# Performance work log

Measured on AMD Instinct MI355X. Metric: run time of the kernel, lower is better.

The kernel has to match this reference:

```python
import jax, jax.numpy as jnp
import numpy as np

B, T, D = 4, 2048, 1024
H, Dh = 16, 64
Q_LAT, KV_LAT, O_LAT = 512, 256, 512
ROPE = 32
FFN_RANK, FFN_INTER = 384, 4096
EPS = 1e-6
THETA = 10000.0


def rms_norm(x, w, eps=EPS):
    xf = x.astype(jnp.float32)
    var = jnp.mean(xf * xf, axis=-1, keepdims=True)
    return (w * (xf * jax.lax.rsqrt(var + eps))).astype(x.dtype)


def rotate_half(x):
    x1, x2 = jnp.split(x, 2, axis=-1)
    return jnp.concatenate([-x2, x1], axis=-1)


def setup_inputs() -> dict:
    key = jax.random.key(0)
    ks = jax.random.split(key, 12)
    s = lambda fan_in: 1.0 / np.sqrt(fan_in)
    inp = {
        "hidden_states": jax.random.normal(ks[0], (B, T, D), jnp.float32),
        "ln1_w": jnp.ones((D,), jnp.float32),
        "a_ln_w": jnp.ones((Q_LAT + KV_LAT,), jnp.float32),
        "qkv_a_w": jax.random.normal(ks[1], (D, Q_LAT + KV_LAT), jnp.float32) * s(D),
        "q_b_w": jax.random.normal(ks[2], (Q_LAT, H * Dh), jnp.float32) * s(Q_LAT),
        "kv_b_w": jax.random.normal(ks[3], (KV_LAT, 2 * H * Dh), jnp.float32) * s(KV_LAT),
        "o_a_w": jax.random.normal(ks[4], (H * Dh, O_LAT), jnp.float32) * s(H * Dh),
        "o_b_w": jax.random.normal(ks[5], (O_LAT, D), jnp.float32) * s(O_LAT),
        "ln2_w": jnp.ones((D,), jnp.float32),
        "ffn_in_a": jax.random.normal(ks[6], (D, FFN_RANK), jnp.float32) * s(D),
        "ffn_in_b": jax.random.normal(ks[7], (FFN_RANK, FFN_INTER), jnp.float32) * s(FFN_RANK),
        "ffn_out_a": jax.random.normal(ks[8], (FFN_INTER, FFN_RANK), jnp.float32) * s(FFN_INTER),
        "ffn_out_b": jax.random.normal(ks[9], (FFN_RANK, D), jnp.float32) * s(FFN_RANK),
    }
    # RoPE tables over first ROPE dims of each head
    inv_freq = 1.0 / (THETA ** (np.arange(0, ROPE, 2, dtype=np.float32) / ROPE))
    t = np.arange(T, dtype=np.float32)
    freqs = np.outer(t, inv_freq)                      # [T, ROPE/2]
    emb = np.concatenate([freqs, freqs], axis=-1)      # [T, ROPE]
    inp["cos"] = jnp.asarray(np.cos(emb), jnp.float32)
    inp["sin"] = jnp.asarray(np.sin(emb), jnp.float32)
    return inp


def reference(hidden_states, cos, sin, ln1_w, a_ln_w, qkv_a_w, q_b_w, kv_b_w,
              o_a_w, o_b_w, ln2_w, ffn_in_a, ffn_in_b, ffn_out_a, ffn_out_b):
    x = hidden_states
    # --- MLA attention (pre-norm) ---
    h = rms_norm(x, ln1_w)
    lat = rms_norm(h @ qkv_a_w, a_ln_w)                # [B,T,Q_LAT+KV_LAT]
    q_lat, kv_lat = jnp.split(lat, [Q_LAT], axis=-1)
    q = (q_lat @ q_b_w).reshape(B, T, H, Dh).transpose(0, 2, 1, 3)   # [B,H,T,Dh]
    kv = (kv_lat @ kv_b_w).reshape(B, T, H, 2 * Dh).transpose(0, 2, 1, 3)
    k, v = jnp.split(kv, 2, axis=-1)
    # partial RoPE on first ROPE dims
    c = cos[None, None]; s_ = sin[None, None]          # [1,1,T,ROPE]
    q_r, q_p = q[..., :ROPE], q[..., ROPE:]
    k_r, k_p = k[..., :ROPE], k[..., ROPE:]
    q = jnp.concatenate([q_r * c + rotate_half(q_r) * s_, q_p], axis=-1)
    k = jnp.concatenate([k_r * c + rotate_half(k_r) * s_, k_p], axis=-1)
    scores = jnp.einsum("bhqd,bhkd->bhqk", q, k) * (Dh ** -0.5)
    attn = jax.nn.softmax(scores, axis=-1)
    ctx = jnp.einsum("bhqk,bhkd->bhqd", attn, v)
    ctx = ctx.transpose(0, 2, 1, 3).reshape(B, T, H * Dh)
    attn_out = (ctx @ o_a_w) @ o_b_w                   # output subspace
    x = x + attn_out
    # --- decomposed FFN (pre-norm) ---
    h2 = rms_norm(x, ln2_w)
    ff = jax.nn.gelu((h2 @ ffn_in_a) @ ffn_in_b)
    ff = (ff @ ffn_out_a) @ ffn_out_b
    return x + ff
```

## Files before the change

kernel.cpp:

```cpp
#include <hip/hip_runtime.h>
#include <hip/hip_bf16.h>
#include <stdint.h>

#define NB 4
#define NT 2048
#define ND 1024
#define NH 16
#define NDH 64
#define NQL 512
#define NKVL 256
#define NLAT 768
#define NOLAT 512
#define NFR 384
#define NFI 4096
#define NTOK 8192

typedef unsigned short u16;
typedef __attribute__((ext_vector_type(4))) float f32x4;
typedef __attribute__((ext_vector_type(8))) short s16x8;
typedef __attribute__((ext_vector_type(8))) u16   u16x8;
typedef __attribute__((ext_vector_type(4))) u16   u16x4;

__device__ __forceinline__ float fast_exp2(float x) {
    return __builtin_amdgcn_exp2f(x);
}

__device__ __forceinline__ u16 f2bf(float f) {
    uint32_t u = __float_as_uint(f);
    u = (u + 0x7FFFu + ((u >> 16) & 1u)) >> 16;
    return (u16)u;
}
__device__ __forceinline__ u16 f2bf_fast(float f) {
    return (u16)((__float_as_uint(f) + 0x8000u) >> 16);
}
__device__ __forceinline__ float bf2f(u16 h) {
    return __uint_as_float(((uint32_t)h) << 16);
}

__device__ __forceinline__ void async_cp16(const void* g, void* l) {
    __builtin_amdgcn_global_load_lds(
        (const __attribute__((address_space(1))) void*)g,
        (__attribute__((address_space(3))) void*)l, 16, 0, 0);
}

__device__ __forceinline__ void wait_vm4()   { asm volatile("s_waitcnt vmcnt(4)" ::: "memory"); }
__device__ __forceinline__ void wait_vm0()   { asm volatile("s_waitcnt vmcnt(0)" ::: "memory"); }
__device__ __forceinline__ void wait_lgkm0() { asm volatile("s_waitcnt lgkmcnt(0)" ::: "memory"); }
__device__ __forceinline__ void raw_barrier(){ asm volatile("s_barrier" ::: "memory"); }

struct TDesc { const float* s; u16* d; int K; int N; int tile0; };
struct TPack { TDesc t[9]; };

__global__ __launch_bounds__(256) void k_transpose_all(TPack p)
{
    __shared__ float tile[32][33];
    int bid = blockIdx.x;
    int i = 0;
    #pragma unroll
    for (int j = 1; j < 9; j++) if (bid >= p.t[j].tile0) i = j;
    const float* src = p.t[i].s;
    u16* dst = p.t[i].d;
    int K = p.t[i].K, N = p.t[i].N;
    int local = bid - p.t[i].tile0;
    int nx = N >> 5;
    int n0 = (local % nx) * 32, k0 = (local / nx) * 32;
    int tx = threadIdx.x, ty = threadIdx.y;
    #pragma unroll
    for (int r = 0; r < 32; r += 8)
        tile[ty + r][tx] = src[(size_t)(k0 + ty + r) * N + n0 + tx];
    __syncthreads();
    #pragma unroll
    for (int r = 0; r < 32; r += 8)
        dst[(size_t)(n0 + ty + r) * K + k0 + tx] = f2bf(tile[tx][ty + r]);
}

template<int W>
__global__ __launch_bounds__(256) void k_rmsnorm(
    const float* __restrict__ x, const float* __restrict__ w, u16* __restrict__ out)
{
    constexpr int E = W / 256;
    int row = blockIdx.x, tid = threadIdx.x;
    const float* xr = x + (size_t)row * W;
    float v[E]; float ss = 0.f;
    #pragma unroll
    for (int i = 0; i < E; i++) { v[i] = xr[tid + i * 256]; ss += v[i] * v[i]; }
    #pragma unroll
    for (int m = 1; m < 64; m <<= 1) ss += __shfl_xor(ss, m, 64);
    __shared__ float red[4];
    if ((tid & 63) == 0) red[tid >> 6] = ss;
    __syncthreads();
    ss = red[0] + red[1] + red[2] + red[3];
    float scale = rsqrtf(ss / (float)W + 1e-6f);
    u16* orow = out + (size_t)row * W;
    #pragma unroll
    for (int i = 0; i < E; i++)
        orow[tid + i * 256] = f2bf(w[tid + i * 256] * (v[i] * scale));
}

template<int EPI>
__global__ __launch_bounds__(256) void k_gemm(
    const u16* __restrict__ A, int lda,
    const u16* __restrict__ Bt,
    int M, int N, int K,
    float* __restrict__ outF, u16* __restrict__ outB,
    const float* __restrict__ resid)
{
    __shared__ __align__(16) u16 As[2][4096];
    __shared__ __align__(16) u16 Bs[2][4096];
    int tid = threadIdx.x;
    int w = tid >> 6, lane = tid & 63;
    int m0 = blockIdx.y * 128, n0 = blockIdx.x * 128;
    int wm = w & 1, wn = w >> 1;
    int lr = lane & 15, lq = lane >> 4;

    f32x4 acc[4][4];
    #pragma unroll
    for (int i = 0; i < 4; i++)
        #pragma unroll
        for (int j = 0; j < 4; j++) acc[i][j] = (f32x4)(0.f);

    int ar = tid >> 2;
    int ac = (tid & 3) * 8;
    const u16* Ag = A  + (size_t)(m0 + ar) * lda + ac;
    const u16* Bg = Bt + (size_t)(n0 + ar) * K   + ac;
    int lo = w * 512;

    auto stage = [&](int kt, int s) {
        const u16* a  = Ag + (size_t)kt * 32;
        const u16* bp = Bg + (size_t)kt * 32;
        async_cp16(a,                     &As[s][lo]);
        async_cp16(a + (size_t)64 * lda,  &As[s][lo + 2048]);
        async_cp16(bp,                    &Bs[s][lo]);
        async_cp16(bp + (size_t)64 * K,   &Bs[s][lo + 2048]);
    };

    int nk = K >> 5;
    stage(0, 0);
    stage(1, 1);
    for (int k = 0; k < nk; k++) {
        if (k + 1 < nk) wait_vm4(); else wait_vm0();
        raw_barrier();
        int s = k & 1;
        s16x8 af[4], bfr[4];
        #pragma unroll
        for (int ms = 0; ms < 4; ms++)
            af[ms] = *reinterpret_cast<const s16x8*>(&As[s][(wm * 64 + ms * 16 + lr) * 32 + lq * 8]);
        #pragma unroll
        for (int ns = 0; ns < 4; ns++)
            bfr[ns] = *reinterpret_cast<const s16x8*>(&Bs[s][(wn * 64 + ns * 16 + lr) * 32 + lq * 8]);
        #pragma unroll
        for (int ms = 0; ms < 4; ms++)
            #pragma unroll
            for (int ns = 0; ns < 4; ns++)
                acc[ms][ns] = __builtin_amdgcn_mfma_f32_16x16x32_bf16(af[ms], bfr[ns], acc[ms][ns], 0, 0, 0);
        wait_lgkm0();
        raw_barrier();
        if (k + 2 < nk) stage(k + 2, s);
    }

    #pragma unroll
    for (int ms = 0; ms < 4; ms++) {
        #pragma unroll
        for (int ns = 0; ns < 4; ns++) {
            int col = n0 + wn * 64 + ns * 16 + lr;
            #pragma unroll
            for (int r = 0; r < 4; r++) {
                int row = m0 + wm * 64 + ms * 16 + lq * 4 + r;
                float v = acc[ms][ns][r];
                size_t idx = (size_t)row * N + col;
                if (EPI == 0) {
                    outF[idx] = v;
                } else if (EPI == 1) {
                    outB[idx] = f2bf(v);
                } else if (EPI == 2) {
                    float t = 0.7978845608028654f * (v + 0.044715f * v * v * v);
                    outB[idx] = f2bf(0.5f * v * (1.f + tanhf(t)));
                } else {
                    outF[idx] = v + resid[idx];
                }
            }
        }
    }
}

__global__ __launch_bounds__(256) void k_rope(
    const u16* __restrict__ q, const u16* __restrict__ kv,
    const float* __restrict__ cosb, const float* __restrict__ sinb,
    u16* __restrict__ q_r, u16* __restrict__ k_r)
{
    const float QS = 0.125f * 1.4426950408889634f;
    int idx = blockIdx.x * 256 + threadIdx.x;
    int g = idx & 7;
    int h = (idx >> 3) & 15;
    int t = (idx >> 7) & 2047;
    int b = idx >> 18;
    size_t qsrc = ((size_t)((b * 2048 + t) * 16 + h)) * 64 + g * 8;
    size_t ksrc = ((size_t)((b * 2048 + t) * 16 + h)) * 128 + g * 8;
    u16x8 qa = *(const u16x8*)&q[qsrc];
    u16x8 ka = *(const u16x8*)&kv[ksrc];
    u16x8 qo, ko;
    if (g < 4) {
        int pd = ((g ^ 2) - g) * 8;
        u16x8 qp = *(const u16x8*)&q[qsrc + pd];
        u16x8 kp = *(const u16x8*)&kv[ksrc + pd];
        float sgn = (g < 2) ? -1.f : 1.f;
        const float* cp = &cosb[t * 32 + g * 8];
        const float* sp = &sinb[t * 32 + g * 8];
        #pragma unroll
        for (int j = 0; j < 8; j++) {
            float c = cp[j], s = sp[j];
            qo[j] = f2bf((bf2f(qa[j]) * c + sgn * bf2f(qp[j]) * s) * QS);
            ko[j] = f2bf(bf2f(ka[j]) * c + sgn * bf2f(kp[j]) * s);
        }
    } else {
        #pragma unroll
        for (int j = 0; j < 8; j++) {
            qo[j] = f2bf(bf2f(qa[j]) * QS);
            ko[j] = ka[j];
        }
    }
    size_t dst = ((size_t)(b * 16 + h) * 2048 + t) * 64 + g * 8;
    *(u16x8*)&q_r[dst] = qo;
    *(u16x8*)&k_r[dst] = ko;
}

__global__ __launch_bounds__(256) void k_vtrans(
    const u16* __restrict__ kv, u16* __restrict__ v_t)
{
    __shared__ u16 tile[64][72];
    int bh = blockIdx.y;
    int b = bh >> 4, h = bh & 15;
    int t0 = blockIdx.x * 64;
    int tid = threadIdx.x;
    int r = tid >> 2;
    int c4 = (tid & 3) * 16;
    const u16* src = kv + ((size_t)((b * 2048 + t0 + r) * 16 + h)) * 128 + 64;
    #pragma unroll
    for (int j = 0; j < 16; j += 8)
        *(u16x8*)&tile[r][c4 + j] = *(const u16x8*)&src[c4 + j];
    __syncthreads();
    int dd = tid >> 2;
    u16* dst = v_t + ((size_t)bh * 64 + dd) * 2048 + t0;
    #pragma unroll
    for (int j0 = 0; j0 < 16; j0 += 8) {
        u16x8 vv;
        #pragma unroll
        for (int j = 0; j < 8; j++) vv[j] = tile[c4 + j0 + j][dd];
        *(u16x8*)&dst[c4 + j0] = vv;
    }
}

__global__ __launch_bounds__(256) void k_attn(
    const u16* __restrict__ q_r, const u16* __restrict__ k_r,
    const u16* __restrict__ v_t, u16* __restrict__ ctx)
{
    __shared__ __align__(16) u16 Ks[4096];
    __shared__ __align__(16) u16 Vs[4096];
    __shared__ __align__(16) u16 Ps[4][2048];
    int tid = threadIdx.x, w = tid >> 6, lane = tid & 63;
    int bh = blockIdx.y;
    int b = bh >> 4, h = bh & 15;
    int q0 = blockIdx.x * 128 + w * 32;
    const u16* Qp = q_r + (size_t)bh * 2048 * 64;
    const u16* Kp = k_r + (size_t)bh * 2048 * 64;
    const u16* Vp = v_t + (size_t)bh * 64 * 2048;
    int lr = lane & 15, lq = lane >> 4;
    int rot = (lr * 8) & 63;

    s16x8 qf[2][2];
    #pragma unroll
    for (int qc = 0; qc < 2; qc++)
        #pragma unroll
        for (int kf = 0; kf < 2; kf++)
            qf[qc][kf] = *(const s16x8*)&Qp[(size_t)(q0 + qc * 16 + lr) * 64 + kf * 32 + lq * 8];

    const u16* gstage;
    u16* lstage;
    size_t grow;
    if (w < 2) {
        gstage = Kp + (size_t)(lane >> 2) * 64 + w * 32 + (lane & 3) * 8;
        lstage = Ks + w * 2048;
        grow = 16 * 64;
    } else {
        gstage = Vp + (size_t)(lane >> 2) * 2048 + (w - 2) * 32 + (lane & 3) * 8;
        lstage = Vs + (w - 2) * 2048;
        grow = 16 * 2048;
    }

    float l0 = 0.f, l1 = 0.f;
    f32x4 o[2][4];
    #pragma unroll
    for (int qt = 0; qt < 2; qt++)
        #pragma unroll
        for (int ds = 0; ds < 4; ds++) o[qt][ds] = (f32x4)(0.f);

    u16* Pw = Ps[w];

    for (int kt = 0; kt < 2048; kt += 64) {
        size_t goff = (w < 2) ? (size_t)kt * 64 : (size_t)kt;
        #pragma unroll
        for (int g = 0; g < 4; g++)
            async_cp16(gstage + goff + g * grow, lstage + g * 512);
        __syncthreads();

        f32x4 sc[2][4];
        #pragma unroll
        for (int ns = 0; ns < 4; ns++) {
            s16x8 a0 = *(const s16x8*)&Ks[(ns * 16 + lr) * 32 + lq * 8];
            s16x8 a1 = *(const s16x8*)&Ks[2048 + (ns * 16 + lr) * 32 + lq * 8];
            #pragma unroll
            for (int qc = 0; qc < 2; qc++) {
                f32x4 t = (f32x4)(0.f);
                t = __builtin_amdgcn_mfma_f32_16x16x32_bf16(a0, qf[qc][0], t, 0, 0, 0);
                t = __builtin_amdgcn_mfma_f32_16x16x32_bf16(a1, qf[qc][1], t, 0, 0, 0);
                sc[qc][ns] = t;
            }
        }

        float rs0 = 0.f, rs1 = 0.f;
        #pragma unroll
        for (int ns = 0; ns < 4; ns++) {
            u16x4 pk0, pk1;
            #pragma unroll
            for (int r = 0; r < 4; r++) {
                float p0 = fast_exp2(sc[0][ns][r]);
                float p1 = fast_exp2(sc[1][ns][r]);
                rs0 += p0; rs1 += p1;
                pk0[r] = f2bf_fast(p0);
                pk1[r] = f2bf_fast(p1);
            }
            int c0 = (ns * 16 + lq * 4 + rot) & 63;
            *(u16x4*)&Pw[lr * 64 + c0] = pk0;
            *(u16x4*)&Pw[(16 + lr) * 64 + c0] = pk1;
        }
        rs0 += __shfl_xor(rs0, 16, 64);
        rs0 += __shfl_xor(rs0, 32, 64);
        rs1 += __shfl_xor(rs1, 16, 64);
        rs1 += __shfl_xor(rs1, 32, 64);
        l0 += rs0;
        l1 += rs1;

        #pragma unroll
        for (int kf = 0; kf < 2; kf++) {
            int cr = (kf * 32 + lq * 8 + rot) & 63;
            s16x8 pf0 = *(const s16x8*)&Pw[lr * 64 + cr];
            s16x8 pf1 = *(const s16x8*)&Pw[(16 + lr) * 64 + cr];
            #pragma unroll
            for (int ds = 0; ds < 4; ds++) {
                s16x8 vf = *(const s16x8*)&Vs[kf * 2048 + (ds * 16 + lr) * 32 + lq * 8];
                o[0][ds] = __builtin_amdgcn_mfma_f32_16x16x32_bf16(pf0, vf, o[0][ds], 0, 0, 0);
                o[1][ds] = __builtin_amdgcn_mfma_f32_16x16x32_bf16(pf1, vf, o[1][ds], 0, 0, 0);
            }
        }
        __syncthreads();
    }

    #pragma unroll
    for (int qt = 0; qt < 2; qt++) {
        float lv = qt ? l1 : l0;
        float li[4];
        #pragma unroll
        for (int r = 0; r < 4; r++) li[r] = 1.f / __shfl(lv, lq * 4 + r, 64);
        #pragma unroll
        for (int ds = 0; ds < 4; ds++)
            #pragma unroll
            for (int r = 0; r < 4; r++) {
                int tq = q0 + qt * 16 + lq * 4 + r;
                float v = o[qt][ds][r] * li[r];
                ctx[((size_t)(b * 2048) + tq) * 1024 + h * 64 + ds * 16 + lr] = f2bf(v);
            }
    }
}

extern "C" void kernel_launch(void* const* d_in, const int* in_sizes, int n_in,
                              void* d_out, int out_size, void* d_ws, size_t ws_size,
                              hipStream_t stream) {
    (void)in_sizes; (void)n_in; (void)out_size; (void)ws_size;
    const float* x     = (const float*)d_in[0];
    const float* ln1   = (const float*)d_in[1];
    const float* alnw  = (const float*)d_in[2];
    const float* qkv_a = (const float*)d_in[3];
    const float* q_b   = (const float*)d_in[4];
    const float* kv_b  = (const float*)d_in[5];
    const float* o_a   = (const float*)d_in[6];
    const float* o_b   = (const float*)d_in[7];
    const float* ln2   = (const float*)d_in[8];
    const float* in_a  = (const float*)d_in[9];
    const float* in_b  = (const float*)d_in[10];
    const float* out_a = (const float*)d_in[11];
    const float* out_b = (const float*)d_in[12];
    const float* cosb  = (const float*)d_in[13];
    const float* sinb  = (const float*)d_in[14];
    float* out = (float*)d_out;
    char* ws = (char*)d_ws;

    u16* wqkv = (u16*)(ws);
    u16* wq   = wqkv + 786432;
    u16* wkv  = wq   + 524288;
    u16* woa  = wkv  + 524288;
    u16* wob  = woa  + 524288;
    u16* wia  = wob  + 524288;
    u16* wib  = wia  + 393216;
    u16* woa2 = wib  + 1572864;
    u16* wob2 = woa2 + 1572864;

    float* x2 = (float*)(ws + 13631488);
    char* P = ws + 47185920;
    u16*  hbuf    = (u16*)(P + 0);
    float* lat_raw = (float*)(P + 16777216);
    u16*  lat     = (u16*)(P + 41943040);
    u16*  qbuf    = (u16*)(P + 54525952);
    u16*  kvbuf   = (u16*)(P + 71303168);
    u16*  q_r     = (u16*)(P + 0);
    u16*  k_r     = (u16*)(P + 16777216);
    u16*  v_t     = (u16*)(P + 33554432);
    u16*  ctx     = (u16*)(P + 54525952);
    u16*  t_oa    = (u16*)(P + 71303168);
    u16*  h2      = (u16*)(P + 79691776);
    u16*  t1      = (u16*)(P + 96468992);
    u16*  t2      = (u16*)(P + 0);
    u16*  t3      = (u16*)(P + 67108864);

    TPack tp;
    tp.t[0] = { qkv_a, wqkv, 1024, 768,  0 };
    tp.t[1] = { q_b,   wq,   512,  1024, 768 };
    tp.t[2] = { kv_b,  wkv,  256,  2048, 1280 };
    tp.t[3] = { o_a,   woa,  1024, 512,  1792 };
    tp.t[4] = { o_b,   wob,  512,  1024, 2304 };
    tp.t[5] = { in_a,  wia,  1024, 384,  2816 };
    tp.t[6] = { in_b,  wib,  384,  4096, 3200 };
    tp.t[7] = { out_a, woa2, 4096, 384,  4736 };
    tp.t[8] = { out_b, wob2, 384,  1024, 6272 };
    k_transpose_all<<<6656, dim3(32, 8), 0, stream>>>(tp);

    k_rmsnorm<1024><<<NTOK, 256, 0, stream>>>(x, ln1, hbuf);
    k_gemm<0><<<dim3(6, 64),  256, 0, stream>>>(hbuf, 1024, wqkv, NTOK, 768, 1024, lat_raw, nullptr, nullptr);
    k_rmsnorm<768><<<NTOK, 256, 0, stream>>>(lat_raw, alnw, lat);
    k_gemm<1><<<dim3(8, 64),  256, 0, stream>>>(lat,       768, wq,  NTOK, 1024, 512, nullptr, qbuf,  nullptr);
    k_gemm<1><<<dim3(16, 64), 256, 0, stream>>>(lat + 512, 768, wkv, NTOK, 2048, 256, nullptr, kvbuf, nullptr);
    k_rope<<<4096, 256, 0, stream>>>(qbuf, kvbuf, cosb, sinb, q_r, k_r);
    k_vtrans<<<dim3(32, 64), 256, 0, stream>>>(kvbuf, v_t);
    k_attn<<<dim3(16, 64), 256, 0, stream>>>(q_r, k_r, v_t, ctx);
    k_gemm<1><<<dim3(4, 64),  256, 0, stream>>>(ctx,  1024, woa,  NTOK, 512, 1024, nullptr, t_oa, nullptr);
    k_gemm<3><<<dim3(8, 64),  256, 0, stream>>>(t_oa, 512,  wob,  NTOK, 1024, 512, x2, nullptr, x);
    k_rmsnorm<1024><<<NTOK, 256, 0, stream>>>(x2, ln2, h2);
    k_gemm<1><<<dim3(3, 64),  256, 0, stream>>>(h2, 1024, wia,  NTOK, 384, 1024, nullptr, t1, nullptr);
    k_gemm<2><<<dim3(32, 64), 256, 0, stream>>>(t1, 384,  wib,  NTOK, 4096, 384, nullptr, t2, nullptr);
    k_gemm<1><<<dim3(3, 64),  256, 0, stream>>>(t2, 4096, woa2, NTOK, 384, 4096, nullptr, t3, nullptr);
    k_gemm<3><<<dim3(8, 64),  256, 0, stream>>>(t3, 384,  wob2, NTOK, 1024, 384, out, nullptr, x2);
}
```

Baseline: 562.6 us.

## Fold attention output projections, split-K GEMMs, chunk FFN, double-buffer attention KV

Precomputes the product of o_a and o_b once so the attention output becomes a single 1024x1024 GEMM instead of two chained GEMMs. Adds split-K via blockIdx.z with atomic float accumulation for the narrow-N GEMMs (qkv_a, ffn_in_a, ffn_out_a), using a memset plus conversion kernels. Splits the FFN intermediate into two 2048-wide chunks so the GELU output fits in a smaller, more cache-friendly buffer. Double-buffers the K/V tiles in the attention kernel with async loads. Atomics make the results nondeterministic and change rounding, the folded weight is rounded to bf16 once more, and extra kernels and a memset are added.

```diff
diff --git a/kernel.cpp b/kernel.cpp
--- a/kernel.cpp
+++ b/kernel.cpp
@@ -2,17 +2,6 @@
 #include <hip/hip_bf16.h>
 #include <stdint.h>
 
-#define NB 4
-#define NT 2048
-#define ND 1024
-#define NH 16
-#define NDH 64
-#define NQL 512
-#define NKVL 256
-#define NLAT 768
-#define NOLAT 512
-#define NFR 384
-#define NFI 4096
 #define NTOK 8192
 
 typedef unsigned short u16;
@@ -24,7 +13,6 @@
 __device__ __forceinline__ float fast_exp2(float x) {
     return __builtin_amdgcn_exp2f(x);
 }
-
 __device__ __forceinline__ u16 f2bf(float f) {
     uint32_t u = __float_as_uint(f);
     u = (u + 0x7FFFu + ((u >> 16) & 1u)) >> 16;
@@ -36,20 +24,18 @@
 __device__ __forceinline__ float bf2f(u16 h) {
     return __uint_as_float(((uint32_t)h) << 16);
 }
-
 __device__ __forceinline__ void async_cp16(const void* g, void* l) {
     __builtin_amdgcn_global_load_lds(
         (const __attribute__((address_space(1))) void*)g,
         (__attribute__((address_space(3))) void*)l, 16, 0, 0);
 }
-
 __device__ __forceinline__ void wait_vm4()   { asm volatile("s_waitcnt vmcnt(4)" ::: "memory"); }
 __device__ __forceinline__ void wait_vm0()   { asm volatile("s_waitcnt vmcnt(0)" ::: "memory"); }
 __device__ __forceinline__ void wait_lgkm0() { asm volatile("s_waitcnt lgkmcnt(0)" ::: "memory"); }
 __device__ __forceinline__ void raw_barrier(){ asm volatile("s_barrier" ::: "memory"); }
 
 struct TDesc { const float* s; u16* d; int K; int N; int tile0; };
-struct TPack { TDesc t[9]; };
+struct TPack { TDesc t[8]; };
 
 __global__ __launch_bounds__(256) void k_transpose_all(TPack p)
 {
@@ -57,7 +43,7 @@
     int bid = blockIdx.x;
     int i = 0;
     #pragma unroll
-    for (int j = 1; j < 9; j++) if (bid >= p.t[j].tile0) i = j;
+    for (int j = 1; j < 8; j++) if (bid >= p.t[j].tile0) i = j;
     const float* src = p.t[i].s;
     u16* dst = p.t[i].d;
     int K = p.t[i].K, N = p.t[i].N;
@@ -74,6 +60,17 @@
         dst[(size_t)(n0 + ty + r) * K + k0 + tx] = f2bf(tile[tx][ty + r]);
 }
 
+__global__ __launch_bounds__(256) void k_cvt(
+    const float* __restrict__ in, u16* __restrict__ out)
+{
+    int i = (blockIdx.x * 256 + threadIdx.x) * 4;
+    f32x4 v = *(const f32x4*)&in[i];
+    u16x4 o;
+    #pragma unroll
+    for (int j = 0; j < 4; j++) o[j] = f2bf(v[j]);
+    *(u16x4*)&out[i] = o;
+}
+
 template<int W>
 __global__ __launch_bounds__(256) void k_rmsnorm(
     const float* __restrict__ x, const float* __restrict__ w, u16* __restrict__ out)
@@ -100,7 +97,7 @@
 template<int EPI>
 __global__ __launch_bounds__(256) void k_gemm(
     const u16* __restrict__ A, int lda,
-    const u16* __restrict__ Bt,
+    const u16* __restrict__ Bt, int ldb,
     int M, int N, int K,
     float* __restrict__ outF, u16* __restrict__ outB,
     const float* __restrict__ resid)
@@ -112,6 +109,7 @@
     int m0 = blockIdx.y * 128, n0 = blockIdx.x * 128;
     int wm = w & 1, wn = w >> 1;
     int lr = lane & 15, lq = lane >> 4;
+    int koff = blockIdx.z * K;
 
     f32x4 acc[4][4];
     #pragma unroll
@@ -121,17 +119,17 @@
 
     int ar = tid >> 2;
     int ac = (tid & 3) * 8;
-    const u16* Ag = A  + (size_t)(m0 + ar) * lda + ac;
-    const u16* Bg = Bt + (size_t)(n0 + ar) * K   + ac;
+    const u16* Ag = A  + (size_t)(m0 + ar) * lda + ac + koff;
+    const u16* Bg = Bt + (size_t)(n0 + ar) * ldb + ac + koff;
     int lo = w * 512;
 
     auto stage = [&](int kt, int s) {
-        const u16* a  = Ag + (size_t)kt * 32;
-        const u16* bp = Bg + (size_t)kt * 32;
+        const u16* a  = Ag + kt * 32;
+        const u16* bp = Bg + kt * 32;
         async_cp16(a,                     &As[s][lo]);
         async_cp16(a + (size_t)64 * lda,  &As[s][lo + 2048]);
         async_cp16(bp,                    &Bs[s][lo]);
-        async_cp16(bp + (size_t)64 * K,   &Bs[s][lo + 2048]);
+        async_cp16(bp + (size_t)64 * ldb, &Bs[s][lo + 2048]);
     };
 
     int nk = K >> 5;
@@ -168,15 +166,15 @@
                 int row = m0 + wm * 64 + ms * 16 + lq * 4 + r;
                 float v = acc[ms][ns][r];
                 size_t idx = (size_t)row * N + col;
-                if (EPI == 0) {
-                    outF[idx] = v;
-                } else if (EPI == 1) {
+                if (EPI == 1) {
                     outB[idx] = f2bf(v);
                 } else if (EPI == 2) {
                     float t = 0.7978845608028654f * (v + 0.044715f * v * v * v);
                     outB[idx] = f2bf(0.5f * v * (1.f + tanhf(t)));
+                } else if (EPI == 3) {
+                    outF[idx] = v + resid[idx];
                 } else {
-                    outF[idx] = v + resid[idx];
+                    unsafeAtomicAdd(&outF[idx], v);
                 }
             }
         }
@@ -254,8 +252,8 @@
     const u16* __restrict__ q_r, const u16* __restrict__ k_r,
     const u16* __restrict__ v_t, u16* __restrict__ ctx)
 {
-    __shared__ __align__(16) u16 Ks[4096];
-    __shared__ __align__(16) u16 Vs[4096];
+    __shared__ __align__(16) u16 Ks[2][4096];
+    __shared__ __align__(16) u16 Vs[2][4096];
     __shared__ __align__(16) u16 Ps[4][2048];
     int tid = threadIdx.x, w = tid >> 6, lane = tid & 63;
     int bh = blockIdx.y;
@@ -275,17 +273,24 @@
             qf[qc][kf] = *(const s16x8*)&Qp[(size_t)(q0 + qc * 16 + lr) * 64 + kf * 32 + lq * 8];
 
     const u16* gstage;
-    u16* lstage;
+    u16 *lp0, *lp1;
     size_t grow;
     if (w < 2) {
         gstage = Kp + (size_t)(lane >> 2) * 64 + w * 32 + (lane & 3) * 8;
-        lstage = Ks + w * 2048;
+        lp0 = &Ks[0][w * 2048]; lp1 = &Ks[1][w * 2048];
         grow = 16 * 64;
     } else {
         gstage = Vp + (size_t)(lane >> 2) * 2048 + (w - 2) * 32 + (lane & 3) * 8;
-        lstage = Vs + (w - 2) * 2048;
+        lp0 = &Vs[0][(w - 2) * 2048]; lp1 = &Vs[1][(w - 2) * 2048];
         grow = 16 * 2048;
     }
+    auto stage = [&](int kt, int s) {
+        size_t goff = (w < 2) ? (size_t)kt * 64 : (size_t)kt;
+        u16* lp = s ? lp1 : lp0;
+        #pragma unroll
+        for (int g = 0; g < 4; g++)
+            async_cp16(gstage + goff + g * grow, lp + g * 512);
+    };
 
     float l0 = 0.f, l1 = 0.f;
     f32x4 o[2][4];
@@ -296,18 +301,20 @@
 
     u16* Pw = Ps[w];
 
-    for (int kt = 0; kt < 2048; kt += 64) {
-        size_t goff = (w < 2) ? (size_t)kt * 64 : (size_t)kt;
-        #pragma unroll
-        for (int g = 0; g < 4; g++)
-            async_cp16(gstage + goff + g * grow, lstage + g * 512);
-        __syncthreads();
+    stage(0, 0);
+    stage(64, 1);
+    for (int k = 0; k < 32; k++) {
+        if (k < 31) wait_vm4(); else wait_vm0();
+        raw_barrier();
+        int s = k & 1;
+        const u16* Ksb = Ks[s];
+        const u16* Vsb = Vs[s];
 
         f32x4 sc[2][4];
         #pragma unroll
         for (int ns = 0; ns < 4; ns++) {
-            s16x8 a0 = *(const s16x8*)&Ks[(ns * 16 + lr) * 32 + lq * 8];
-            s16x8 a1 = *(const s16x8*)&Ks[2048 + (ns * 16 + lr) * 32 + lq * 8];
+            s16x8 a0 = *(const s16x8*)&Ksb[(ns * 16 + lr) * 32 + lq * 8];
+            s16x8 a1 = *(const s16x8*)&Ksb[2048 + (ns * 16 + lr) * 32 + lq * 8];
             #pragma unroll
             for (int qc = 0; qc < 2; qc++) {
                 f32x4 t = (f32x4)(0.f);
@@ -347,12 +354,14 @@
             s16x8 pf1 = *(const s16x8*)&Pw[(16 + lr) * 64 + cr];
             #pragma unroll
             for (int ds = 0; ds < 4; ds++) {
-                s16x8 vf = *(const s16x8*)&Vs[kf * 2048 + (ds * 16 + lr) * 32 + lq * 8];
+                s16x8 vf = *(const s16x8*)&Vsb[kf * 2048 + (ds * 16 + lr) * 32 + lq * 8];
                 o[0][ds] = __builtin_amdgcn_mfma_f32_16x16x32_bf16(pf0, vf, o[0][ds], 0, 0, 0);
                 o[1][ds] = __builtin_amdgcn_mfma_f32_16x16x32_bf16(pf1, vf, o[1][ds], 0, 0, 0);
             }
         }
-        __syncthreads();
+        wait_lgkm0();
+        raw_barrier();
+        if (k + 2 < 32) stage((k + 2) * 64, s);
     }
 
     #pragma unroll
@@ -394,58 +403,65 @@
     float* out = (float*)d_out;
     char* ws = (char*)d_ws;
 
-    u16* wqkv = (u16*)(ws);
+    u16* wqkv = (u16*)ws;
     u16* wq   = wqkv + 786432;
     u16* wkv  = wq   + 524288;
-    u16* woa  = wkv  + 524288;
-    u16* wob  = woa  + 524288;
+    u16* wob  = wkv  + 524288;
     u16* wia  = wob  + 524288;
     u16* wib  = wia  + 393216;
     u16* woa2 = wib  + 1572864;
     u16* wob2 = woa2 + 1572864;
-
-    float* x2 = (float*)(ws + 13631488);
-    char* P = ws + 47185920;
-    u16*  hbuf    = (u16*)(P + 0);
-    float* lat_raw = (float*)(P + 16777216);
-    u16*  lat     = (u16*)(P + 41943040);
-    u16*  qbuf    = (u16*)(P + 54525952);
-    u16*  kvbuf   = (u16*)(P + 71303168);
-    u16*  q_r     = (u16*)(P + 0);
-    u16*  k_r     = (u16*)(P + 16777216);
-    u16*  v_t     = (u16*)(P + 33554432);
-    u16*  ctx     = (u16*)(P + 54525952);
-    u16*  t_oa    = (u16*)(P + 71303168);
-    u16*  h2      = (u16*)(P + 79691776);
-    u16*  t1      = (u16*)(P + 96468992);
-    u16*  t2      = (u16*)(P + 0);
-    u16*  t3      = (u16*)(P + 67108864);
+    u16* woan = wob2 + 393216;
+    u16* woab = woan + 524288;
+    float* lat_raw = (float*)(ws + 15728640);
+    float* t1f     = (float*)(ws + 40894464);
+    float* t3f     = (float*)(ws + 53477376);
+    char* G = ws + 66060288;
+    u16*  hbuf  = (u16*)(G + 0);
+    u16*  lat   = (u16*)(G + 16777216);
+    u16*  qbuf  = (u16*)(G + 29360128);
+    u16*  kvbuf = (u16*)(G + 46137344);
+    u16*  q_r   = (u16*)(G + 0);
+    u16*  k_r   = (u16*)(ws + 15728640);
+    u16*  v_t   = (u16*)(G + 16777216);
+    u16*  ctx   = (u16*)(G + 33554432);
+    float* x2   = (float*)(G + 50331648);
+    u16*  h2    = (u16*)(G + 0);
+    u16*  t1    = (u16*)(G + 16777216);
+    u16*  t2h   = (u16*)(ws + 15728640);
+    u16*  t3    = (u16*)(G + 23068672);
+
+    hipMemsetAsync(ws + 15728640, 0, 50331648, stream);
 
     TPack tp;
     tp.t[0] = { qkv_a, wqkv, 1024, 768,  0 };
     tp.t[1] = { q_b,   wq,   512,  1024, 768 };
     tp.t[2] = { kv_b,  wkv,  256,  2048, 1280 };
-    tp.t[3] = { o_a,   woa,  1024, 512,  1792 };
-    tp.t[4] = { o_b,   wob,  512,  1024, 2304 };
-    tp.t[5] = { in_a,  wia,  1024, 384,  2816 };
-    tp.t[6] = { in_b,  wib,  384,  4096, 3200 };
-    tp.t[7] = { out_a, woa2, 4096, 384,  4736 };
-    tp.t[8] = { out_b, wob2, 384,  1024, 6272 };
-    k_transpose_all<<<6656, dim3(32, 8), 0, stream>>>(tp);
+    tp.t[3] = { o_b,   wob,  512,  1024, 1792 };
+    tp.t[4] = { in_a,  wia,  1024, 384,  2304 };
+    tp.t[5] = { in_b,  wib,  384,  4096, 2688 };
+    tp.t[6] = { out_a, woa2, 4096, 384,  4224 };
+    tp.t[7] = { out_b, wob2, 384,  1024, 5760 };
+    k_transpose_all<<<6144, dim3(32, 8), 0, stream>>>(tp);
+    k_cvt<<<512, 256, 0, stream>>>(o_a, woan);
+    k_gemm<1><<<dim3(8, 8, 1), 256, 0, stream>>>(wob, 512, woan, 512, 1024, 1024, 512, nullptr, woab, nullptr);
 
     k_rmsnorm<1024><<<NTOK, 256, 0, stream>>>(x, ln1, hbuf);
-    k_gemm<0><<<dim3(6, 64),  256, 0, stream>>>(hbuf, 1024, wqkv, NTOK, 768, 1024, lat_raw, nullptr, nullptr);
+    k_gemm<4><<<dim3(6, 64, 2), 256, 0, stream>>>(hbuf, 1024, wqkv, 1024, NTOK, 768, 512, lat_raw, nullptr, nullptr);
     k_rmsnorm<768><<<NTOK, 256, 0, stream>>>(lat_raw, alnw, lat);
-    k_gemm<1><<<dim3(8, 64),  256, 0, stream>>>(lat,       768, wq,  NTOK, 1024, 512, nullptr, qbuf,  nullptr);
-    k_gemm<1><<<dim3(16, 64), 256, 0, stream>>>(lat + 512, 768, wkv, NTOK, 2048, 256, nullptr, kvbuf, nullptr);
+    k_gemm<1><<<dim3(8, 64, 1),  256, 0, stream>>>(lat,       768, wq,  512, NTOK, 1024, 512, nullptr, qbuf,  nullptr);
+    k_gemm<1><<<dim3(16, 64, 1), 256, 0, stream>>>(lat + 512, 768, wkv, 256, NTOK, 2048, 256, nullptr, kvbuf, nullptr);
     k_rope<<<4096, 256, 0, stream>>>(qbuf, kvbuf, cosb, sinb, q_r, k_r);
     k_vtrans<<<dim3(32, 64), 256, 0, stream>>>(kvbuf, v_t);
     k_attn<<<dim3(16, 64), 256, 0, stream>>>(q_r, k_r, v_t, ctx);
-    k_gemm<1><<<dim3(4, 64),  256, 0, stream>>>(ctx,  1024, woa,  NTOK, 512, 1024, nullptr, t_oa, nullptr);
-    k_gemm<3><<<dim3(8, 64),  256, 0, stream>>>(t_oa, 512,  wob,  NTOK, 1024, 512, x2, nullptr, x);
+    k_gemm<3><<<dim3(8, 64, 1), 256, 0, stream>>>(ctx, 1024, woab, 1024, NTOK, 1024, 1024, x2, nullptr, x);
     k_rmsnorm<1024><<<NTOK, 256, 0, stream>>>(x2, ln2, h2);
-    k_gemm<1><<<dim3(3, 64),  256, 0, stream>>>(h2, 1024, wia,  NTOK, 384, 1024, nullptr, t1, nullptr);
-    k_gemm<2><<<dim3(32, 64), 256, 0, stream>>>(t1, 384,  wib,  NTOK, 4096, 384, nullptr, t2, nullptr);
-    k_gemm<1><<<dim3(3, 64),  256, 0, stream>>>(t2, 4096, woa2, NTOK, 384, 4096, nullptr, t3, nullptr);
-    k_gemm<3><<<dim3(8, 64),  256, 0, stream>>>(t3, 384,  wob2, NTOK, 1024, 384, out, nullptr, x2);
-}
+    k_gemm<4><<<dim3(3, 64, 2), 256, 0, stream>>>(h2, 1024, wia, 1024, NTOK, 384, 512, t1f, nullptr, nullptr);
+    k_cvt<<<3072, 256, 0, stream>>>(t1f, t1);
+    k_gemm<2><<<dim3(16, 64, 1), 256, 0, stream>>>(t1, 384, wib,              384, NTOK, 2048, 384, nullptr, t2h, nullptr);
+    k_gemm<4><<<dim3(3, 64, 2),  256, 0, stream>>>(t2h, 2048, woa2,          4096, NTOK, 384, 1024, t3f, nullptr, nullptr);
+    k_gemm<2><<<dim3(16, 64, 1), 256, 0, stream>>>(t1, 384, wib + 2048 * 384, 384, NTOK, 2048, 384, nullptr, t2h, nullptr);
+    k_gemm<4><<<dim3(3, 64, 2),  256, 0, stream>>>(t2h, 2048, woa2 + 2048,   4096, NTOK, 384, 1024, t3f, nullptr, nullptr);
+    k_cvt<<<3072, 256, 0, stream>>>(t3f, t3);
+    k_gemm<3><<<dim3(8, 64, 1), 256, 0, stream>>>(t3, 384, wob2, 384, NTOK, 1024, 384, out, nullptr, x2);
+}
```

After: 635.8 us. 13.0% more time.
